# Kernel tuning notes

Measured on AMD Instinct MI355X. Metric: run time of the kernel, lower is better.

## Reference

```python
import jax, jax.numpy as jnp
import numpy as np

RANK = 8
A_SHAPE = (64, 128)   # (a1, a2)
B_SHAPE = (16, 32)    # (b1, b2)
BATCH = 16384


def setup_inputs() -> dict:
    key = jax.random.key(0)
    k1, k2, k3, k4, k5 = jax.random.split(key, 5)
    a1, a2 = A_SHAPE
    b1, b2 = B_SHAPE
    x = jax.random.normal(k1, (BATCH, a1 * b1), dtype=jnp.float32)
    # xavier-uniform style init for a and b (as in nn.init.xavier_uniform_)
    lim_a = float(np.sqrt(6.0 / (a1 + a2)))
    lim_b = float(np.sqrt(6.0 / (b1 + b2)))
    a = jax.random.uniform(k2, (RANK, a1, a2), minval=-lim_a, maxval=lim_a, dtype=jnp.float32)
    b = jax.random.uniform(k3, (RANK, b1, b2), minval=-lim_b, maxval=lim_b, dtype=jnp.float32)
    s = jax.random.normal(k4, (a1, a2), dtype=jnp.float32)          # structured-sparse mask
    bias = jax.random.normal(k5, (a2 * b2,), dtype=jnp.float32)     # bias_shape[1:] = (a2*b2,)
    return {"x": x, "a": a, "b": b, "s": s, "bias": bias}


def reference(x, a, b, s, bias):
    # structured-sparse elementwise mask on a
    a_eff = s[None, :, :] * a                          # (rank, a1, a2)
    r, a1, a2 = a_eff.shape
    _, b1, b2 = b.shape
    # w = sum_r kron(a_eff[r], b[r]) : (a1*b1, a2*b2)
    w = jnp.einsum('rij,rkl->ikjl', a_eff, b).reshape(a1 * b1, a2 * b2)
    out = x @ w                                        # (batch, a2*b2)
    return out + bias[None, :]
```

## Files before the change

kernel.cpp:

```cpp
#include <hip/hip_runtime.h>
#include <hip/hip_bf16.h>

typedef short bf16x8 __attribute__((ext_vector_type(8)));
typedef float f32x4 __attribute__((ext_vector_type(4)));

static constexpr int M_DIM = 16384;
static constexpr int N_DIM = 4096;
static constexpr int K_DIM = 1024;

static constexpr int CVT_BLOCKS = (M_DIM * K_DIM / 8) / 256;
static constexpr int WT_BLOCKS  = N_DIM;

__device__ __forceinline__ unsigned short f2bf(float f) {
  union { float f; unsigned u; } v; v.f = f;
  unsigned r = v.u + 0x7FFFu + ((v.u >> 16) & 1u);
  return (unsigned short)(r >> 16);
}

__global__ __launch_bounds__(256) void prep_kernel(
    const float* __restrict__ x, const float* __restrict__ a,
    const float* __restrict__ b, const float* __restrict__ s,
    unsigned short* __restrict__ xb, unsigned short* __restrict__ wT) {
  __shared__ float as_eff[8][64];
  __shared__ float bl[8][16];
  const int tid = threadIdx.x;

  if (blockIdx.x < CVT_BLOCKS) {
    const int i = (blockIdx.x * 256 + tid) * 2;
    float4 v0 = reinterpret_cast<const float4*>(x)[i];
    float4 v1 = reinterpret_cast<const float4*>(x)[i + 1];
    ushort4 o0, o1;
    o0.x = f2bf(v0.x); o0.y = f2bf(v0.y); o0.z = f2bf(v0.z); o0.w = f2bf(v0.w);
    o1.x = f2bf(v1.x); o1.y = f2bf(v1.y); o1.z = f2bf(v1.z); o1.w = f2bf(v1.w);
    reinterpret_cast<ushort4*>(xb)[i] = o0;
    reinterpret_cast<ushort4*>(xb)[i + 1] = o1;
    return;
  }

  const int n = blockIdx.x - CVT_BLOCKS;
  const int j = n >> 5, l = n & 31;

#pragma unroll
  for (int t = tid; t < 512; t += 256) {
    const int r = t >> 6, i = t & 63;
    as_eff[r][i] = a[(r * 64 + i) * 128 + j] * s[i * 128 + j];
  }
  if (tid < 128) {
    const int r = tid >> 4, kk = tid & 15;
    bl[r][kk] = b[(r * 16 + kk) * 32 + l];
  }
  __syncthreads();

  const int i = tid >> 2;
  const int kk0 = (tid & 3) * 4;
  float o[4] = {0.f, 0.f, 0.f, 0.f};
#pragma unroll
  for (int r = 0; r < 8; ++r) {
    const float av = as_eff[r][i];
#pragma unroll
    for (int q = 0; q < 4; ++q)
      o[q] += av * bl[r][kk0 + q];
  }
  ushort4 w4;
  w4.x = f2bf(o[0]); w4.y = f2bf(o[1]); w4.z = f2bf(o[2]); w4.w = f2bf(o[3]);
  *reinterpret_cast<ushort4*>(&wT[(size_t)n * K_DIM + tid * 4]) = w4;
}


#define PH_BARRIER __builtin_amdgcn_s_barrier()
#define SCHED0     __builtin_amdgcn_sched_barrier(0)
#define WAITV(N)   do { asm volatile("s_waitcnt vmcnt(" #N ")" ::: "memory"); SCHED0; } while (0)
#define WAITL(N)   do { asm volatile("s_waitcnt lgkmcnt(" #N ")" ::: "memory"); SCHED0; } while (0)

__device__ __forceinline__ void quad_mfma(f32x4 (&acc)[8][4], const bf16x8 (&aH)[4][2],
                                          const bf16x8 (&bH)[2][2], int mbase, int nbase) {
  __builtin_amdgcn_s_setprio(1);
#pragma unroll
  for (int ks = 0; ks < 2; ++ks)
#pragma unroll
    for (int mi = 0; mi < 4; ++mi)
#pragma unroll
      for (int ni = 0; ni < 2; ++ni)
        acc[mbase + mi][nbase + ni] = __builtin_amdgcn_mfma_f32_16x16x32_bf16(
            aH[mi][ks], bH[ni][ks], acc[mbase + mi][nbase + ni], 0, 0, 0);
  __builtin_amdgcn_s_setprio(0);
}

__global__ __launch_bounds__(512, 2) void gemm8_kernel(
    const unsigned short* __restrict__ A, const unsigned short* __restrict__ BT,
    const float* __restrict__ bias, float* __restrict__ C) {
  __shared__ __align__(16) unsigned short Al[2][16384];
  __shared__ __align__(16) unsigned short Bl[2][16384];

  const int tid  = threadIdx.x;
  const int lane = tid & 63;
  const int wave = tid >> 6;
  const int wm = wave >> 2;
  const int wn = wave & 3;
  const int wr = wm * 128;
  const int wc = wn * 64;
  const int frow = lane & 15;
  const int kg = lane >> 4;
  const int swz0 = (kg * 16) ^ ((lane & 7) << 4);
  const int swz1 = (64 + kg * 16) ^ ((lane & 7) << 4);

  int bid = blockIdx.x;
  int gid = bid >> 4, lid = bid & 15;
  gid = ((gid & 7) << 3) | (gid >> 3);
  const int bm = (gid >> 2) * 4 + (lid >> 2);
  const int bn = (gid & 3) * 4 + (lid & 3);
  const int brow = bm * 256, bcol = bn * 256;

  const unsigned short* Abase = A + (size_t)brow * K_DIM;
  const unsigned short* Bbase = BT + (size_t)bcol * K_DIM;

  const int srow = tid >> 3;
  const int scol = ((((tid & 7) << 4) ^ ((srow & 7) << 4)) >> 1);
  const int ldsu = __builtin_amdgcn_readfirstlane(wave * 512);

#define STG(dst, base, q, k0) __builtin_amdgcn_global_load_lds( \
    (const __attribute__((address_space(1))) void*)((base) + (size_t)((q)*64 + srow) * K_DIM + (k0) + scol), \
    (__attribute__((address_space(3))) void*)((dst) + (q)*4096 + ldsu), 16, 0, 0)

#define LOAD_AH(P, h) { _Pragma("unroll") for (int mi = 0; mi < 4; ++mi) { \
    const char* p_ = (const char*)(P) + (wr + frow + ((h)*4 + mi) * 16) * 128; \
    aF[mi][0] = *(const bf16x8*)(p_ + swz0); aF[mi][1] = *(const bf16x8*)(p_ + swz1); } }

#define LOAD_BH(P, h, dst) { _Pragma("unroll") for (int ni = 0; ni < 2; ++ni) { \
    const char* p_ = (const char*)(P) + (wc + frow + ((h)*2 + ni) * 16) * 128; \
    dst[ni][0] = *(const bf16x8*)(p_ + swz0); dst[ni][1] = *(const bf16x8*)(p_ + swz1); } }

  f32x4 acc[8][4] = {};
  bf16x8 aF[4][2], b0[2][2], b1[2][2];

  STG(Bl[0], Bbase, 0, 0);  STG(Bl[0], Bbase, 1, 0);
  STG(Bl[0], Bbase, 2, 0);  STG(Bl[0], Bbase, 3, 0);
  STG(Al[0], Abase, 0, 0);  STG(Al[0], Abase, 1, 0);
  STG(Al[0], Abase, 2, 0);  STG(Al[0], Abase, 3, 0);
  STG(Bl[1], Bbase, 0, 64); STG(Bl[1], Bbase, 1, 64);
  STG(Bl[1], Bbase, 2, 64); STG(Bl[1], Bbase, 3, 64);
  WAITV(4);
  PH_BARRIER;

  unsigned short* a_rd = &Al[0][0]; unsigned short* a_st = &Al[1][0];
  unsigned short* b_rd = &Bl[0][0]; unsigned short* b_st = &Bl[1][0];

#pragma unroll 1
  for (int t = 0; t < 16; ++t) {
    const int k = t * 64;
    LOAD_AH(a_rd, 0); SCHED0;
    LOAD_BH(b_rd, 0, b0); SCHED0;
    if (t < 15) { STG(a_st, Abase, 0, k + 64); STG(a_st, Abase, 1, k + 64); }
    WAITL(8);
    PH_BARRIER;
    WAITL(0);
    quad_mfma(acc, aF, b0, 0, 0);
    PH_BARRIER;
    LOAD_BH(b_rd, 1, b1); SCHED0;
    if (t < 15) { STG(a_st, Abase, 2, k + 64); STG(a_st, Abase, 3, k + 64); }
    PH_BARRIER;
    WAITL(0);
    quad_mfma(acc, aF, b1, 0, 2);
    PH_BARRIER;
    LOAD_AH(a_rd, 1); SCHED0;
    if (t < 14) { STG(b_rd, Bbase, 0, k + 128); STG(b_rd, Bbase, 1, k + 128); }
    PH_BARRIER;
    WAITL(0);
    quad_mfma(acc, aF, b1, 4, 2);
    PH_BARRIER;
    if (t < 14) { STG(b_rd, Bbase, 2, k + 128); STG(b_rd, Bbase, 3, k + 128); }
    PH_BARRIER;
    quad_mfma(acc, aF, b0, 4, 0);
    if (t < 14) { WAITV(4); } else if (t == 14) { WAITV(0); }
    PH_BARRIER;
    unsigned short* tp = a_rd; a_rd = a_st; a_st = tp;
    tp = b_rd; b_rd = b_st; b_st = tp;
  }

  __syncthreads();
  float* T = (float*)&Al[0][0];
  float* Tw = T + wave * (16 * 68);
  const int col4 = lane & 15;
  const int rsel = lane >> 4;
  float4 bv = *(const float4*)&bias[bcol + wc + col4 * 4];

#pragma unroll
  for (int mi = 0; mi < 8; ++mi) {
#pragma unroll
    for (int ni = 0; ni < 4; ++ni)
#pragma unroll
      for (int r = 0; r < 4; ++r)
        Tw[(kg * 4 + r) * 68 + ni * 16 + frow] = acc[mi][ni][r];
    WAITL(0);
#pragma unroll
    for (int rr = 0; rr < 4; ++rr) {
      float4 v = *(float4*)&Tw[(rr * 4 + rsel) * 68 + col4 * 4];
      v.x += bv.x; v.y += bv.y; v.z += bv.z; v.w += bv.w;
      *(float4*)&C[(size_t)(brow + wr + mi * 16 + rr * 4 + rsel) * N_DIM + bcol + wc + col4 * 4] = v;
    }
    WAITL(0);
  }
}

extern "C" void kernel_launch(void* const* d_in, const int* in_sizes, int n_in,
                              void* d_out, int out_size, void* d_ws, size_t ws_size,
                              hipStream_t stream) {
  const float* x    = (const float*)d_in[0];
  const float* a    = (const float*)d_in[1];
  const float* b    = (const float*)d_in[2];
  const float* s    = (const float*)d_in[3];
  const float* bias = (const float*)d_in[4];
  float* out = (float*)d_out;

  unsigned short* xb = (unsigned short*)d_ws;
  unsigned short* wT = (unsigned short*)((char*)d_ws + (size_t)M_DIM * K_DIM * 2);

  prep_kernel<<<CVT_BLOCKS + WT_BLOCKS, 256, 0, stream>>>(x, a, b, s, xb, wT);
  gemm8_kernel<<<(M_DIM / 256) * (N_DIM / 256), 512, 0, stream>>>(xb, wT, bias, out);
}
```

Baseline: 188.1 us.

## Shrink GEMM tile to 256x128 with 4 waves and K-step of 32

```diff
diff --git a/kernel.cpp b/kernel.cpp
--- a/kernel.cpp
+++ b/kernel.cpp
@@ -72,109 +72,89 @@
 #define WAITV(N)   do { asm volatile("s_waitcnt vmcnt(" #N ")" ::: "memory"); SCHED0; } while (0)
 #define WAITL(N)   do { asm volatile("s_waitcnt lgkmcnt(" #N ")" ::: "memory"); SCHED0; } while (0)
 
-__device__ __forceinline__ void quad_mfma(f32x4 (&acc)[8][4], const bf16x8 (&aH)[4][2],
-                                          const bf16x8 (&bH)[2][2], int mbase, int nbase) {
-  __builtin_amdgcn_s_setprio(1);
-#pragma unroll
-  for (int ks = 0; ks < 2; ++ks)
-#pragma unroll
-    for (int mi = 0; mi < 4; ++mi)
-#pragma unroll
-      for (int ni = 0; ni < 2; ++ni)
-        acc[mbase + mi][nbase + ni] = __builtin_amdgcn_mfma_f32_16x16x32_bf16(
-            aH[mi][ks], bH[ni][ks], acc[mbase + mi][nbase + ni], 0, 0, 0);
-  __builtin_amdgcn_s_setprio(0);
-}
-
-__global__ __launch_bounds__(512, 2) void gemm8_kernel(
+__global__ __launch_bounds__(256, 2) void gemm_kernel(
     const unsigned short* __restrict__ A, const unsigned short* __restrict__ BT,
     const float* __restrict__ bias, float* __restrict__ C) {
-  __shared__ __align__(16) unsigned short Al[2][16384];
-  __shared__ __align__(16) unsigned short Bl[2][16384];
+  __shared__ __align__(16) unsigned short Al[2][8192];
+  __shared__ __align__(16) unsigned short Bl[2][4096];
 
   const int tid  = threadIdx.x;
   const int lane = tid & 63;
   const int wave = tid >> 6;
-  const int wm = wave >> 2;
-  const int wn = wave & 3;
+  const int wm = wave >> 1;
+  const int wn = wave & 1;
   const int wr = wm * 128;
   const int wc = wn * 64;
   const int frow = lane & 15;
   const int kg = lane >> 4;
-  const int swz0 = (kg * 16) ^ ((lane & 7) << 4);
-  const int swz1 = (64 + kg * 16) ^ ((lane & 7) << 4);
+  const int swz = (kg ^ ((frow >> 1) & 3)) << 4;
 
   int bid = blockIdx.x;
-  int gid = bid >> 4, lid = bid & 15;
-  gid = ((gid & 7) << 3) | (gid >> 3);
-  const int bm = (gid >> 2) * 4 + (lid >> 2);
-  const int bn = (gid & 3) * 4 + (lid & 3);
-  const int brow = bm * 256, bcol = bn * 256;
+  int g = bid >> 4, lid = bid & 15;
+  g = ((g & 7) << 4) | (g >> 3);
+  const int bm = (g >> 3) * 4 + (lid >> 2);
+  const int bn = (g & 7) * 4 + (lid & 3);
+  const int brow = bm * 256, bcol = bn * 128;
 
   const unsigned short* Abase = A + (size_t)brow * K_DIM;
   const unsigned short* Bbase = BT + (size_t)bcol * K_DIM;
 
-  const int srow = tid >> 3;
-  const int scol = ((((tid & 7) << 4) ^ ((srow & 7) << 4)) >> 1);
+  const int srow = tid >> 2;
+  const int schunk = ((tid & 3) ^ ((tid >> 3) & 3)) * 8;
   const int ldsu = __builtin_amdgcn_readfirstlane(wave * 512);
 
 #define STG(dst, base, q, k0) __builtin_amdgcn_global_load_lds( \
-    (const __attribute__((address_space(1))) void*)((base) + (size_t)((q)*64 + srow) * K_DIM + (k0) + scol), \
-    (__attribute__((address_space(3))) void*)((dst) + (q)*4096 + ldsu), 16, 0, 0)
-
-#define LOAD_AH(P, h) { _Pragma("unroll") for (int mi = 0; mi < 4; ++mi) { \
-    const char* p_ = (const char*)(P) + (wr + frow + ((h)*4 + mi) * 16) * 128; \
-    aF[mi][0] = *(const bf16x8*)(p_ + swz0); aF[mi][1] = *(const bf16x8*)(p_ + swz1); } }
-
-#define LOAD_BH(P, h, dst) { _Pragma("unroll") for (int ni = 0; ni < 2; ++ni) { \
-    const char* p_ = (const char*)(P) + (wc + frow + ((h)*2 + ni) * 16) * 128; \
-    dst[ni][0] = *(const bf16x8*)(p_ + swz0); dst[ni][1] = *(const bf16x8*)(p_ + swz1); } }
+    (const __attribute__((address_space(1))) void*)((base) + (size_t)((q)*64 + srow) * K_DIM + (k0) + schunk), \
+    (__attribute__((address_space(3))) void*)((dst) + (q)*2048 + ldsu), 16, 0, 0)
+
+#define STGA(dst, k0) do { STG(dst, Abase, 0, k0); STG(dst, Abase, 1, k0); \
+                           STG(dst, Abase, 2, k0); STG(dst, Abase, 3, k0); } while (0)
+#define STGB(dst, k0) do { STG(dst, Bbase, 0, k0); STG(dst, Bbase, 1, k0); } while (0)
+
+#define LDA4(P, h) { _Pragma("unroll") for (int mi = 0; mi < 4; ++mi) \
+    aF[(h)*4 + mi] = *(const bf16x8*)((const char*)(P) + (wr + ((h)*4 + mi) * 16 + frow) * 64 + swz); }
+#define LDB2(P, h) { _Pragma("unroll") for (int ni = 0; ni < 2; ++ni) \
+    bF[(h)*2 + ni] = *(const bf16x8*)((const char*)(P) + (wc + ((h)*2 + ni) * 16 + frow) * 64 + swz); }
+
+#define MFMA_C(mlo, mcnt, nlo, ncnt) do { __builtin_amdgcn_s_setprio(1); \
+    _Pragma("unroll") for (int mi = 0; mi < (mcnt); ++mi) \
+    _Pragma("unroll") for (int ni = 0; ni < (ncnt); ++ni) \
+      acc[(mlo)+mi][(nlo)+ni] = __builtin_amdgcn_mfma_f32_16x16x32_bf16( \
+          aF[(mlo)+mi], bF[(nlo)+ni], acc[(mlo)+mi][(nlo)+ni], 0, 0, 0); \
+    __builtin_amdgcn_s_setprio(0); } while (0)
 
   f32x4 acc[8][4] = {};
-  bf16x8 aF[4][2], b0[2][2], b1[2][2];
-
-  STG(Bl[0], Bbase, 0, 0);  STG(Bl[0], Bbase, 1, 0);
-  STG(Bl[0], Bbase, 2, 0);  STG(Bl[0], Bbase, 3, 0);
-  STG(Al[0], Abase, 0, 0);  STG(Al[0], Abase, 1, 0);
-  STG(Al[0], Abase, 2, 0);  STG(Al[0], Abase, 3, 0);
-  STG(Bl[1], Bbase, 0, 64); STG(Bl[1], Bbase, 1, 64);
-  STG(Bl[1], Bbase, 2, 64); STG(Bl[1], Bbase, 3, 64);
-  WAITV(4);
+  bf16x8 aF[8], bF[4];
+
+  STGB(Bl[0], 0);
+  STGA(Al[0], 0);
+  STGB(Bl[1], 32);
+  WAITV(2);
   PH_BARRIER;
 
   unsigned short* a_rd = &Al[0][0]; unsigned short* a_st = &Al[1][0];
-  unsigned short* b_rd = &Bl[0][0]; unsigned short* b_st = &Bl[1][0];
+  unsigned short* b_rd = &Bl[0][0]; unsigned short* b_ot = &Bl[1][0];
 
 #pragma unroll 1
-  for (int t = 0; t < 16; ++t) {
-    const int k = t * 64;
-    LOAD_AH(a_rd, 0); SCHED0;
-    LOAD_BH(b_rd, 0, b0); SCHED0;
-    if (t < 15) { STG(a_st, Abase, 0, k + 64); STG(a_st, Abase, 1, k + 64); }
-    WAITL(8);
+  for (int t = 0; t < 32; ++t) {
+    const int k = t * 32;
+    LDA4(a_rd, 0); SCHED0;
+    LDB2(b_rd, 0); SCHED0;
+    if (t < 31) STGA(a_st, k + 32);
+    LDA4(a_rd, 1); SCHED0;
+    LDB2(b_rd, 1); SCHED0;
+    WAITL(6);
+    MFMA_C(0, 4, 0, 2);
+    WAITL(2);
+    MFMA_C(4, 4, 0, 2);
+    WAITL(0);
     PH_BARRIER;
-    WAITL(0);
-    quad_mfma(acc, aF, b0, 0, 0);
-    PH_BARRIER;
-    LOAD_BH(b_rd, 1, b1); SCHED0;
-    if (t < 15) { STG(a_st, Abase, 2, k + 64); STG(a_st, Abase, 3, k + 64); }
-    PH_BARRIER;
-    WAITL(0);
-    quad_mfma(acc, aF, b1, 0, 2);
-    PH_BARRIER;
-    LOAD_AH(a_rd, 1); SCHED0;
-    if (t < 14) { STG(b_rd, Bbase, 0, k + 128); STG(b_rd, Bbase, 1, k + 128); }
-    PH_BARRIER;
-    WAITL(0);
-    quad_mfma(acc, aF, b1, 4, 2);
-    PH_BARRIER;
-    if (t < 14) { STG(b_rd, Bbase, 2, k + 128); STG(b_rd, Bbase, 3, k + 128); }
-    PH_BARRIER;
-    quad_mfma(acc, aF, b0, 4, 0);
-    if (t < 14) { WAITV(4); } else if (t == 14) { WAITV(0); }
+    if (t < 30) STGB(b_rd, k + 64);
+    MFMA_C(0, 8, 2, 2);
+    if (t < 30) { WAITV(2); } else if (t == 30) { WAITV(0); }
     PH_BARRIER;
     unsigned short* tp = a_rd; a_rd = a_st; a_st = tp;
-    tp = b_rd; b_rd = b_st; b_st = tp;
+    tp = b_rd; b_rd = b_ot; b_ot = tp;
   }
 
   __syncthreads();
@@ -216,5 +196,5 @@
   unsigned short* wT = (unsigned short*)((char*)d_ws + (size_t)M_DIM * K_DIM * 2);
 
   prep_kernel<<<CVT_BLOCKS + WT_BLOCKS, 256, 0, stream>>>(x, a, b, s, xb, wT);
-  gemm8_kernel<<<(M_DIM / 256) * (N_DIM / 256), 512, 0, stream>>>(xb, wT, bias, out);
-}
+  gemm_kernel<<<(M_DIM / 256) * (N_DIM / 128), 256, 0, stream>>>(xb, wT, bias, out);
+}
```

Result: slower. 197.9 us (+5.2%).
